# Optimization experiments

Measured on AMD Instinct MI355X. Metric: run time of the kernel, lower is better.

## Reference

```python
import jax, jax.numpy as jnp
import numpy as np

EPS = 1e-5
NEG_SLOPE = 0.01  # torch LeakyReLU default


def setup_inputs() -> dict:
    key = jax.random.key(0)
    k1, k2 = jax.random.split(key)
    B, C, N, OUT = 4, 256, 4096, 256
    stdv = 1.0 / np.sqrt(OUT)
    x = jax.random.normal(k1, (B, C, N), dtype=jnp.float32)
    W = jax.random.uniform(k2, (C, OUT), dtype=jnp.float32, minval=-stdv, maxval=stdv)
    gamma = jnp.ones((OUT,), dtype=jnp.float32)
    beta = jnp.zeros((OUT,), dtype=jnp.float32)
    return {"x": x, "W": W, "gamma": gamma, "beta": beta}


def reference(x, W, gamma, beta):
    # x: [B, C, N] -> xt: [B, N, C]
    xt = jnp.transpose(x, (0, 2, 1))
    # adjacency: softmax over last dim of [B, N, N] self-similarity (L2=False path)
    scores = jnp.einsum('bnc,bmc->bnm', xt, xt)
    adj = jax.nn.softmax(scores, axis=-1)
    # support: [B, N, OUT]
    support = jnp.einsum('bnc,co->bno', xt, W)
    # output: [B, OUT, N]
    out = jnp.transpose(jnp.einsum('bnm,bmo->bno', adj, support), (0, 2, 1))
    y = jnp.where(out >= 0, out, NEG_SLOPE * out)  # LeakyReLU
    # BatchNorm1d (training mode): per-channel stats over batch and spatial dims
    mean = jnp.mean(y, axis=(0, 2), keepdims=True)
    var = jnp.mean(jnp.square(y - mean), axis=(0, 2), keepdims=True)
    y_hat = (y - mean) * jax.lax.rsqrt(var + EPS)
    return gamma[None, :, None] * y_hat + beta[None, :, None]
```

## Files before the change

### kernel.cpp

```cpp
#include <hip/hip_runtime.h>

typedef _Float16 f16;
typedef _Float16 f16x2 __attribute__((ext_vector_type(2)));
typedef _Float16 f16x4 __attribute__((ext_vector_type(4)));
typedef _Float16 f16x8 __attribute__((ext_vector_type(8)));
typedef float f32x4 __attribute__((ext_vector_type(4)));
typedef float f32x16 __attribute__((ext_vector_type(16)));
typedef int i32x2 __attribute__((ext_vector_type(2)));

#define B_   4
#define C_   256
#define N_   4096
#define OUT_ 256

__device__ __forceinline__ void gld_lds16(const f16* g, f16* l) {
    __builtin_amdgcn_global_load_lds(
        (const __attribute__((address_space(1))) void*)g,
        (__attribute__((address_space(3))) void*)l, 16, 0, 0);
}

__device__ __forceinline__ i32x2 perm32(float x) {
    return __builtin_amdgcn_permlane32_swap(__float_as_int(x), __float_as_int(x), false, false);
}

__global__ __launch_bounds__(256) void k_prep(const float* __restrict__ x,
                                              const float* __restrict__ W,
                                              f16* __restrict__ xt,
                                              f16* __restrict__ Wt,
                                              float* __restrict__ stats) {
    int bid = blockIdx.x;
    int t = threadIdx.x;
    if (bid < 1024) {
        int b  = bid >> 8;
        int ct = (bid >> 6) & 3;
        int nt = bid & 63;
        int c0 = ct * 64, n0 = nt * 64;
        __shared__ float tile[64][65];
        int nl = t & 63;
        int r0 = t >> 6;
        #pragma unroll
        for (int i = 0; i < 16; ++i) {
            int cl = i * 4 + r0;
            tile[cl][nl] = x[((b * C_ + c0 + cl) * N_) + n0 + nl];
        }
        __syncthreads();
        #pragma unroll
        for (int i = 0; i < 4; ++i) {
            int n  = i * 16 + (t >> 4);
            int c4 = (t & 15) * 4;
            f16x4 o = { (f16)tile[c4][n], (f16)tile[c4 + 1][n],
                        (f16)tile[c4 + 2][n], (f16)tile[c4 + 3][n] };
            *(f16x4*)&xt[((b * N_ + n0 + n) * C_) + c0 + c4] = o;
        }
    } else {
        int wb = bid - 1024;
        #pragma unroll
        for (int i = 0; i < 4; ++i) {
            int idx = wb * 1024 + i * 256 + t;
            int c = idx >> 8, o = idx & 255;
            Wt[o * C_ + c] = (f16)W[idx];
        }
        if (wb < 2) stats[wb * 256 + t] = 0.f;
    }
}

__global__ __launch_bounds__(256) void k_support(const f16* __restrict__ xt,
                                                 const f16* __restrict__ Wt,
                                                 f16* __restrict__ supT) {
    int bid0 = blockIdx.x;
    int bid = (bid0 & 7) * 128 + (bid0 >> 3);
    int b  = bid >> 8;
    int ot = (bid >> 6) & 3;
    int mt = bid & 63;
    int o0 = ot * 64, m0 = mt * 64;
    __shared__ __align__(16) f16 Ws[64][264];
    __shared__ __align__(16) f16 Xs[64][264];
    int t = threadIdx.x;
    int wave = t >> 6, lane = t & 63, q = lane >> 4, l15 = lane & 15;
    #pragma unroll
    for (int p = 0; p < 8; ++p) {
        int idx = p * 256 + t;
        int row = idx >> 5, ch = (idx & 31) * 8;
        *(uint4*)&Ws[row][ch] = *(const uint4*)&Wt[(o0 + row) * C_ + ch];
        *(uint4*)&Xs[row][ch] = *(const uint4*)&xt[((b * N_) + m0 + row) * C_ + ch];
    }
    __syncthreads();
    f32x4 acc[4] = {};
    #pragma unroll
    for (int kk = 0; kk < 8; ++kk) {
        f16x8 a = *(f16x8*)&Ws[16 * wave + l15][kk * 32 + q * 8];
        #pragma unroll
        for (int ct = 0; ct < 4; ++ct) {
            f16x8 bb = *(f16x8*)&Xs[16 * ct + l15][kk * 32 + q * 8];
            acc[ct] = __builtin_amdgcn_mfma_f32_16x16x32_f16(a, bb, acc[ct], 0, 0, 0);
        }
    }
    #pragma unroll
    for (int ct = 0; ct < 4; ++ct)
        #pragma unroll
        for (int r = 0; r < 4; ++r) {
            int og = o0 + 16 * wave + q * 4 + r;
            int mg = m0 + 16 * ct + l15;
            supT[((b * OUT_ + og) * N_) + mg] = (f16)acc[ct][r];
        }
}

__global__ __launch_bounds__(256) __attribute__((amdgpu_waves_per_eu(2, 2)))
void k_flash(const f16* __restrict__ xt,
             const f16* __restrict__ supT,
             f16* __restrict__ Op,
             float* __restrict__ Ml) {
    int bid0 = blockIdx.x;
    int wg = (bid0 & 7) * 64 + (bid0 >> 3);
    int h  = wg >> 8;
    int b  = (wg >> 6) & 3;
    int n0 = (wg & 63) * 64;

    __shared__ __align__(16) f16 KsL[64 * 256];
    __shared__ __align__(16) f16 Ps[64][72];
    __shared__ float Lh[2][64];
    __shared__ float Lt[64];

    int t = threadIdx.x;
    int wave = t >> 6, lane = t & 63;
    int q = lane >> 4, l15 = lane & 15;
    int l31 = lane & 31, hi = lane >> 5;
    int nh = wave & 1, mh = wave >> 1;

    const f16* qbase = xt + ((size_t)(b * N_) + n0 + 32 * nh + l31) * C_ + 8 * hi;
    f16x8 qf[16];
    #pragma unroll
    for (int kc = 0; kc < 16; ++kc)
        qf[kc] = *(const f16x8*)&qbase[16 * kc];

    float m_fix;
    {
        float s = 0.f;
        #pragma unroll
        for (int kc = 0; kc < 16; ++kc)
            #pragma unroll
            for (int j = 0; j < 8; ++j) {
                float v = (float)qf[kc][j];
                s += v * v;
            }
        i32x2 rr = perm32(s);
        m_fix = __int_as_float(rr[0]) + __int_as_float(rr[1]);
    }

    f32x4 oacc[4][4] = {};
    float l_run = 0.f;

    const f16* kbase = xt + (size_t)b * N_ * C_;
    int c16 = (lane & 31) * 8;
    int rhalf = lane >> 5;
    int soff[8];
    #pragma unroll
    for (int j = 0; j < 8; ++j) {
        int row = wave * 16 + j * 2 + rhalf;
        soff[j] = row * 256 + (c16 ^ ((row & 7) << 3));
    }
    int swr = (l31 & 7) << 3;

    const f16* vbbase = supT + ((size_t)(b * OUT_) + 64 * wave + l15) * N_ + q * 8;

    {
        const f16* kt = kbase + (size_t)(h * 2048) * C_;
        #pragma unroll
        for (int j = 0; j < 8; ++j)
            gld_lds16(kt + soff[j], &KsL[wave * 4096 + j * 512]);
    }

    for (int it = 0; it < 32; ++it) {
        int m0 = h * 2048 + it * 64;

        asm volatile("s_waitcnt vmcnt(0) lgkmcnt(0)" ::: "memory");
        __builtin_amdgcn_s_barrier();
        __builtin_amdgcn_sched_barrier(0);

        f16x8 vf[2][4];
        const f16* vb = vbbase + m0;
        #pragma unroll
        for (int ks = 0; ks < 2; ++ks)
            #pragma unroll
            for (int ot = 0; ot < 4; ++ot)
                vf[ks][ot] = *(const f16x8*)&vb[(size_t)(16 * ot) * N_ + ks * 32];

        f32x16 sacc = {};
        const f16* krow = &KsL[(32 * mh + l31) * 256];
        __builtin_amdgcn_s_setprio(1);
        #pragma unroll
        for (int kc = 0; kc < 16; ++kc) {
            int col = (16 * kc + 8 * hi) ^ swr;
            f16x8 kf = *(const f16x8*)&krow[col];
            sacc = __builtin_amdgcn_mfma_f32_32x32x16_f16(kf, qf[kc], sacc, 0, 0, 0);
        }
        __builtin_amdgcn_s_setprio(0);

        float p[16];
        #pragma unroll
        for (int r = 0; r < 16; ++r)
            p[r] = __expf(sacc[r] - m_fix);
        float s0 = (p[0] + p[1]) + (p[2] + p[3]);
        float s1 = (p[4] + p[5]) + (p[6] + p[7]);
        float s2 = (p[8] + p[9]) + (p[10] + p[11]);
        float s3 = (p[12] + p[13]) + (p[14] + p[15]);
        l_run += (s0 + s1) + (s2 + s3);

        #pragma unroll
        for (int g = 0; g < 4; ++g) {
            f16x4 pk = { (f16)p[4 * g], (f16)p[4 * g + 1],
                         (f16)p[4 * g + 2], (f16)p[4 * g + 3] };
            *(f16x4*)&Ps[32 * nh + l31][32 * mh + 8 * g + 4 * hi] = pk;
        }

        asm volatile("s_waitcnt lgkmcnt(0)" ::: "memory");
        __builtin_amdgcn_s_barrier();
        __builtin_amdgcn_sched_barrier(0);

        if (it < 31) {
            const f16* kt = kbase + (size_t)(m0 + 64) * C_;
            #pragma unroll
            for (int j = 0; j < 8; ++j)
                gld_lds16(kt + soff[j], &KsL[wave * 4096 + j * 512]);
        }

        __builtin_amdgcn_s_setprio(1);
        #pragma unroll
        for (int ks = 0; ks < 2; ++ks) {
            f16x8 af[4];
            #pragma unroll
            for (int nt = 0; nt < 4; ++nt)
                af[nt] = *(f16x8*)&Ps[16 * nt + l15][ks * 32 + q * 8];
            #pragma unroll
            for (int nt = 0; nt < 4; ++nt)
                #pragma unroll
                for (int ot = 0; ot < 4; ++ot)
                    oacc[nt][ot] = __builtin_amdgcn_mfma_f32_16x16x32_f16(af[nt], vf[ks][ot], oacc[nt][ot], 0, 0, 0);
        }
        __builtin_amdgcn_s_setprio(0);
    }

    {
        i32x2 rr = perm32(l_run);
        l_run = __int_as_float(rr[0]) + __int_as_float(rr[1]);
    }
    __syncthreads();
    if (lane < 32) Lh[mh][32 * nh + l31] = l_run;
    __syncthreads();
    if (t < 64) {
        float lt = Lh[0][t] + Lh[1][t];
        Lt[t] = 1.0f / fmaxf(lt, 1e-37f);
        Ml[(size_t)wg * 64 + t] = lt;
    }
    __syncthreads();

    float4 lv[4];
    #pragma unroll
    for (int nt = 0; nt < 4; ++nt)
        lv[nt] = *(const float4*)&Lt[16 * nt + 4 * q];

    f16* Obase = Op + (size_t)wg * (64 * 256);
    #pragma unroll
    for (int nt = 0; nt < 4; ++nt)
        #pragma unroll
        for (int ot = 0; ot < 4; ++ot)
            #pragma unroll
            for (int r = 0; r < 4; ++r) {
                int n = 16 * nt + q * 4 + r;
                int o = 64 * wave + 16 * ot + l15;
                Obase[n * 256 + o] = (f16)(oacc[nt][ot][r] * ((const float*)&lv[nt])[r]);
            }
}

__global__ __launch_bounds__(256) void k_merge(const f16* __restrict__ Op,
                                               const float* __restrict__ Ml,
                                               float* __restrict__ out,
                                               float* __restrict__ stats) {
    int bid0 = blockIdx.x;
    int bid = (bid0 & 7) * 128 + (bid0 >> 3);
    int b  = bid >> 8;
    int nb = (bid >> 2) & 63;
    int oq = bid & 3;
    int n0 = nb * 64, o0 = oq * 64;
    int t = threadIdx.x;
    const f16* O1 = Op + (size_t)(b * 64 + nb) * (64 * 256);
    const f16* O2 = Op + (size_t)(b * 64 + nb + 256) * (64 * 256);
    const float* Ml1 = Ml + (size_t)(b * 64 + nb) * 64;
    const float* Ml2 = Ml + (size_t)(b * 64 + nb + 256) * 64;
    __shared__ float c1s[64], c2s[64];
    __shared__ float tile[64][65];
    __shared__ float rs[8][64], rss[8][64];
    if (t < 64) {
        float l1 = Ml1[t], l2 = Ml2[t];
        float inv = 1.0f / (l1 + l2);
        c1s[t] = l1 * inv;
        c2s[t] = l2 * inv;
    }
    __syncthreads();
    int ow = (t & 31) * 2;
    int ng = t >> 5;
    float s0 = 0.f, s1 = 0.f, ss0 = 0.f, ss1 = 0.f;
    #pragma unroll
    for (int j = 0; j < 8; ++j) {
        int n = ng * 8 + j;
        f16x2 u1 = *(const f16x2*)&O1[n * 256 + o0 + ow];
        f16x2 u2 = *(const f16x2*)&O2[n * 256 + o0 + ow];
        float c1 = c1s[n], c2 = c2s[n];
        float v0 = c1 * (float)u1[0] + c2 * (float)u2[0];
        float v1 = c1 * (float)u1[1] + c2 * (float)u2[1];
        v0 = v0 >= 0.f ? v0 : 0.01f * v0;
        v1 = v1 >= 0.f ? v1 : 0.01f * v1;
        s0 += v0; ss0 += v0 * v0;
        s1 += v1; ss1 += v1 * v1;
        tile[ow][n] = v0;
        tile[ow + 1][n] = v1;
    }
    rs[ng][ow] = s0;  rs[ng][ow + 1] = s1;
    rss[ng][ow] = ss0; rss[ng][ow + 1] = ss1;
    __syncthreads();
    if (t < 64) {
        float S = 0.f, SS = 0.f;
        #pragma unroll
        for (int g = 0; g < 8; ++g) { S += rs[g][t]; SS += rss[g][t]; }
        atomicAdd(&stats[o0 + t], S);
        atomicAdd(&stats[256 + o0 + t], SS);
    }
    int w = t >> 6, lane = t & 63;
    float* dst = out + ((size_t)(b * OUT_ + o0)) * N_ + n0;
    #pragma unroll
    for (int k = 0; k < 16; ++k) {
        int o = 16 * w + k;
        dst[(size_t)o * N_ + lane] = tile[o][lane];
    }
}

__global__ __launch_bounds__(256) void k_bnapply(float* __restrict__ y,
                                                 const float* __restrict__ stats,
                                                 const float* __restrict__ gamma,
                                                 const float* __restrict__ beta) {
    int idx = blockIdx.x * 256 + threadIdx.x;
    int o = (idx >> 10) & 255;
    float mean = stats[o] * (1.0f / 16384.0f);
    float var = stats[256 + o] * (1.0f / 16384.0f) - mean * mean;
    float rstd = rsqrtf(var + 1e-5f);
    float g = gamma[o] * rstd;
    float bta = beta[o] - mean * g;
    float4 v = ((const float4*)y)[idx];
    v.x = v.x * g + bta;
    v.y = v.y * g + bta;
    v.z = v.z * g + bta;
    v.w = v.w * g + bta;
    ((float4*)y)[idx] = v;
}

extern "C" void kernel_launch(void* const* d_in, const int* in_sizes, int n_in,
                              void* d_out, int out_size, void* d_ws, size_t ws_size,
                              hipStream_t stream) {
    const float* x     = (const float*)d_in[0];
    const float* W     = (const float*)d_in[1];
    const float* gamma = (const float*)d_in[2];
    const float* beta  = (const float*)d_in[3];
    float* out = (float*)d_out;

    f16* xt    = (f16*)d_ws;
    f16* supT  = xt + (size_t)B_ * N_ * C_;
    f16* Wt    = supT + (size_t)B_ * N_ * OUT_;
    f16* Op    = Wt + C_ * OUT_;
    float* Ml  = (float*)(Op + (size_t)2 * 256 * 64 * 256);
    float* stats = Ml + 512 * 128;

    k_prep<<<1088, 256, 0, stream>>>(x, W, xt, Wt, stats);
    k_support<<<1024, 256, 0, stream>>>(xt, Wt, supT);
    k_flash<<<512, 256, 0, stream>>>(xt, supT, Op, Ml);
    k_merge<<<1024, 256, 0, stream>>>(Op, Ml, out, stats);
    k_bnapply<<<4096, 256, 0, stream>>>(out, stats, gamma, beta);
}
```

Before: 191.6 us.

## Split flash attention keys four ways with workspace-gated fallback double-buffered path

Adds a four-way split-K variant of the flash kernel (1024 blocks over 1024-key halves, waves_per_eu relaxed to 2-4) with a four-way merge kernel, selected when the workspace is large enough. The split aims to improve CU occupancy and load balance on the attention stage. It costs twice the partial-output traffic and a heavier merge. The fallback path keeps the two-way split but double-buffers the K tile in LDS, so the next tile's load overlaps compute.

```diff
diff --git a/kernel.cpp b/kernel.cpp
--- a/kernel.cpp
+++ b/kernel.cpp
@@ -105,13 +105,13 @@
         }
 }
 
-__global__ __launch_bounds__(256) __attribute__((amdgpu_waves_per_eu(2, 2)))
-void k_flash(const f16* __restrict__ xt,
-             const f16* __restrict__ supT,
-             f16* __restrict__ Op,
-             float* __restrict__ Ml) {
+__global__ __launch_bounds__(256) __attribute__((amdgpu_waves_per_eu(2, 4)))
+void k_flash4(const f16* __restrict__ xt,
+              const f16* __restrict__ supT,
+              f16* __restrict__ Op,
+              float* __restrict__ Ml) {
     int bid0 = blockIdx.x;
-    int wg = (bid0 & 7) * 64 + (bid0 >> 3);
+    int wg = (bid0 & 7) * 128 + (bid0 >> 3);
     int h  = wg >> 8;
     int b  = (wg >> 6) & 3;
     int n0 = (wg & 63) * 64;
@@ -164,14 +164,14 @@
     const f16* vbbase = supT + ((size_t)(b * OUT_) + 64 * wave + l15) * N_ + q * 8;
 
     {
-        const f16* kt = kbase + (size_t)(h * 2048) * C_;
+        const f16* kt = kbase + (size_t)(h * 1024) * C_;
         #pragma unroll
         for (int j = 0; j < 8; ++j)
             gld_lds16(kt + soff[j], &KsL[wave * 4096 + j * 512]);
     }
 
-    for (int it = 0; it < 32; ++it) {
-        int m0 = h * 2048 + it * 64;
+    for (int it = 0; it < 16; ++it) {
+        int m0 = h * 1024 + it * 64;
 
         asm volatile("s_waitcnt vmcnt(0) lgkmcnt(0)" ::: "memory");
         __builtin_amdgcn_s_barrier();
@@ -217,7 +217,7 @@
         __builtin_amdgcn_s_barrier();
         __builtin_amdgcn_sched_barrier(0);
 
-        if (it < 31) {
+        if (it < 15) {
             const f16* kt = kbase + (size_t)(m0 + 64) * C_;
             #pragma unroll
             for (int j = 0; j < 8; ++j)
@@ -272,10 +272,246 @@
             }
 }
 
-__global__ __launch_bounds__(256) void k_merge(const f16* __restrict__ Op,
-                                               const float* __restrict__ Ml,
-                                               float* __restrict__ out,
-                                               float* __restrict__ stats) {
+__global__ __launch_bounds__(256) __attribute__((amdgpu_waves_per_eu(2, 2)))
+void k_flash2(const f16* __restrict__ xt,
+              const f16* __restrict__ supT,
+              f16* __restrict__ Op,
+              float* __restrict__ Ml) {
+    int bid0 = blockIdx.x;
+    int wg = (bid0 & 7) * 64 + (bid0 >> 3);
+    int h  = wg >> 8;
+    int b  = (wg >> 6) & 3;
+    int n0 = (wg & 63) * 64;
+
+    __shared__ __align__(16) f16 KsL[2][64 * 256];
+    __shared__ __align__(16) f16 Ps[64][72];
+    __shared__ float Lh[2][64];
+    __shared__ float Lt[64];
+
+    int t = threadIdx.x;
+    int wave = t >> 6, lane = t & 63;
+    int q = lane >> 4, l15 = lane & 15;
+    int l31 = lane & 31, hi = lane >> 5;
+    int nh = wave & 1, mh = wave >> 1;
+
+    const f16* qbase = xt + ((size_t)(b * N_) + n0 + 32 * nh + l31) * C_ + 8 * hi;
+    f16x8 qf[16];
+    #pragma unroll
+    for (int kc = 0; kc < 16; ++kc)
+        qf[kc] = *(const f16x8*)&qbase[16 * kc];
+
+    float m_fix;
+    {
+        float s = 0.f;
+        #pragma unroll
+        for (int kc = 0; kc < 16; ++kc)
+            #pragma unroll
+            for (int j = 0; j < 8; ++j) {
+                float v = (float)qf[kc][j];
+                s += v * v;
+            }
+        i32x2 rr = perm32(s);
+        m_fix = __int_as_float(rr[0]) + __int_as_float(rr[1]);
+    }
+
+    f32x4 oacc[4][4] = {};
+    float l_run = 0.f;
+
+    const f16* kbase = xt + (size_t)b * N_ * C_;
+    int c16 = (lane & 31) * 8;
+    int rhalf = lane >> 5;
+    int soff[8];
+    #pragma unroll
+    for (int j = 0; j < 8; ++j) {
+        int row = wave * 16 + j * 2 + rhalf;
+        soff[j] = row * 256 + (c16 ^ ((row & 7) << 3));
+    }
+    int swr = (l31 & 7) << 3;
+
+    const f16* vbbase = supT + ((size_t)(b * OUT_) + 64 * wave + l15) * N_ + q * 8;
+
+    {
+        const f16* kt = kbase + (size_t)(h * 2048) * C_;
+        #pragma unroll
+        for (int j = 0; j < 8; ++j)
+            gld_lds16(kt + soff[j], &KsL[0][wave * 4096 + j * 512]);
+    }
+
+    int cur = 0;
+    for (int it = 0; it < 32; ++it) {
+        int m0 = h * 2048 + it * 64;
+        __syncthreads();
+
+        f16x8 vf[2][4];
+        const f16* vb = vbbase + m0;
+        #pragma unroll
+        for (int ks = 0; ks < 2; ++ks)
+            #pragma unroll
+            for (int ot = 0; ot < 4; ++ot)
+                vf[ks][ot] = *(const f16x8*)&vb[(size_t)(16 * ot) * N_ + ks * 32];
+
+        if (it < 31) {
+            const f16* kt = kbase + (size_t)(m0 + 64) * C_;
+            #pragma unroll
+            for (int j = 0; j < 8; ++j)
+                gld_lds16(kt + soff[j], &KsL[cur ^ 1][wave * 4096 + j * 512]);
+        }
+
+        f32x16 sacc = {};
+        const f16* krow = &KsL[cur][(32 * mh + l31) * 256];
+        __builtin_amdgcn_s_setprio(1);
+        #pragma unroll
+        for (int kc = 0; kc < 16; ++kc) {
+            int col = (16 * kc + 8 * hi) ^ swr;
+            f16x8 kf = *(const f16x8*)&krow[col];
+            sacc = __builtin_amdgcn_mfma_f32_32x32x16_f16(kf, qf[kc], sacc, 0, 0, 0);
+        }
+        __builtin_amdgcn_s_setprio(0);
+
+        float p[16];
+        #pragma unroll
+        for (int r = 0; r < 16; ++r)
+            p[r] = __expf(sacc[r] - m_fix);
+        float s0 = (p[0] + p[1]) + (p[2] + p[3]);
+        float s1 = (p[4] + p[5]) + (p[6] + p[7]);
+        float s2 = (p[8] + p[9]) + (p[10] + p[11]);
+        float s3 = (p[12] + p[13]) + (p[14] + p[15]);
+        l_run += (s0 + s1) + (s2 + s3);
+
+        #pragma unroll
+        for (int g = 0; g < 4; ++g) {
+            f16x4 pk = { (f16)p[4 * g], (f16)p[4 * g + 1],
+                         (f16)p[4 * g + 2], (f16)p[4 * g + 3] };
+            *(f16x4*)&Ps[32 * nh + l31][32 * mh + 8 * g + 4 * hi] = pk;
+        }
+
+        asm volatile("s_waitcnt lgkmcnt(0)" ::: "memory");
+        __builtin_amdgcn_s_barrier();
+        __builtin_amdgcn_sched_barrier(0);
+
+        __builtin_amdgcn_s_setprio(1);
+        #pragma unroll
+        for (int ks = 0; ks < 2; ++ks) {
+            f16x8 af[4];
+            #pragma unroll
+            for (int nt = 0; nt < 4; ++nt)
+                af[nt] = *(f16x8*)&Ps[16 * nt + l15][ks * 32 + q * 8];
+            #pragma unroll
+            for (int nt = 0; nt < 4; ++nt)
+                #pragma unroll
+                for (int ot = 0; ot < 4; ++ot)
+                    oacc[nt][ot] = __builtin_amdgcn_mfma_f32_16x16x32_f16(af[nt], vf[ks][ot], oacc[nt][ot], 0, 0, 0);
+        }
+        __builtin_amdgcn_s_setprio(0);
+        cur ^= 1;
+    }
+
+    {
+        i32x2 rr = perm32(l_run);
+        l_run = __int_as_float(rr[0]) + __int_as_float(rr[1]);
+    }
+    __syncthreads();
+    if (lane < 32) Lh[mh][32 * nh + l31] = l_run;
+    __syncthreads();
+    if (t < 64) {
+        float lt = Lh[0][t] + Lh[1][t];
+        Lt[t] = 1.0f / fmaxf(lt, 1e-37f);
+        Ml[(size_t)wg * 64 + t] = lt;
+    }
+    __syncthreads();
+
+    float4 lv[4];
+    #pragma unroll
+    for (int nt = 0; nt < 4; ++nt)
+        lv[nt] = *(const float4*)&Lt[16 * nt + 4 * q];
+
+    f16* Obase = Op + (size_t)wg * (64 * 256);
+    #pragma unroll
+    for (int nt = 0; nt < 4; ++nt)
+        #pragma unroll
+        for (int ot = 0; ot < 4; ++ot)
+            #pragma unroll
+            for (int r = 0; r < 4; ++r) {
+                int n = 16 * nt + q * 4 + r;
+                int o = 64 * wave + 16 * ot + l15;
+                Obase[n * 256 + o] = (f16)(oacc[nt][ot][r] * ((const float*)&lv[nt])[r]);
+            }
+}
+
+__global__ __launch_bounds__(256) void k_merge4(const f16* __restrict__ Op,
+                                                const float* __restrict__ Ml,
+                                                float* __restrict__ out,
+                                                float* __restrict__ stats) {
+    int bid0 = blockIdx.x;
+    int bid = (bid0 & 7) * 128 + (bid0 >> 3);
+    int b  = bid >> 8;
+    int nb = (bid >> 2) & 63;
+    int oq = bid & 3;
+    int n0 = nb * 64, o0 = oq * 64;
+    int t = threadIdx.x;
+    const f16* Oh[4];
+    #pragma unroll
+    for (int hh = 0; hh < 4; ++hh)
+        Oh[hh] = Op + (size_t)(hh * 256 + b * 64 + nb) * (64 * 256);
+    __shared__ float cs[4][64];
+    __shared__ float tile[64][65];
+    __shared__ float rs[8][64], rss[8][64];
+    if (t < 64) {
+        float l0 = Ml[(size_t)(0 * 256 + b * 64 + nb) * 64 + t];
+        float l1 = Ml[(size_t)(1 * 256 + b * 64 + nb) * 64 + t];
+        float l2 = Ml[(size_t)(2 * 256 + b * 64 + nb) * 64 + t];
+        float l3 = Ml[(size_t)(3 * 256 + b * 64 + nb) * 64 + t];
+        float inv = 1.0f / (l0 + l1 + l2 + l3);
+        cs[0][t] = l0 * inv;
+        cs[1][t] = l1 * inv;
+        cs[2][t] = l2 * inv;
+        cs[3][t] = l3 * inv;
+    }
+    __syncthreads();
+    int ow = (t & 31) * 2;
+    int ng = t >> 5;
+    float s0 = 0.f, s1 = 0.f, ss0 = 0.f, ss1 = 0.f;
+    #pragma unroll
+    for (int j = 0; j < 8; ++j) {
+        int n = ng * 8 + j;
+        float v0 = 0.f, v1 = 0.f;
+        #pragma unroll
+        for (int hh = 0; hh < 4; ++hh) {
+            f16x2 u = *(const f16x2*)&Oh[hh][n * 256 + o0 + ow];
+            float c = cs[hh][n];
+            v0 += c * (float)u[0];
+            v1 += c * (float)u[1];
+        }
+        v0 = v0 >= 0.f ? v0 : 0.01f * v0;
+        v1 = v1 >= 0.f ? v1 : 0.01f * v1;
+        s0 += v0; ss0 += v0 * v0;
+        s1 += v1; ss1 += v1 * v1;
+        tile[ow][n] = v0;
+        tile[ow + 1][n] = v1;
+    }
+    rs[ng][ow] = s0;  rs[ng][ow + 1] = s1;
+    rss[ng][ow] = ss0; rss[ng][ow + 1] = ss1;
+    __syncthreads();
+    if (t < 64) {
+        float S = 0.f, SS = 0.f;
+        #pragma unroll
+        for (int g = 0; g < 8; ++g) { S += rs[g][t]; SS += rss[g][t]; }
+        atomicAdd(&stats[o0 + t], S);
+        atomicAdd(&stats[256 + o0 + t], SS);
+    }
+    int w = t >> 6, lane = t & 63;
+    float* dst = out + ((size_t)(b * OUT_ + o0)) * N_ + n0;
+    #pragma unroll
+    for (int k = 0; k < 16; ++k) {
+        int o = 16 * w + k;
+        dst[(size_t)o * N_ + lane] = tile[o][lane];
+    }
+}
+
+__global__ __launch_bounds__(256) void k_merge2(const f16* __restrict__ Op,
+                                                const float* __restrict__ Ml,
+                                                float* __restrict__ out,
+                                                float* __restrict__ stats) {
     int bid0 = blockIdx.x;
     int bid = (bid0 & 7) * 128 + (bid0 >> 3);
     int b  = bid >> 8;
@@ -362,16 +598,29 @@
     const float* beta  = (const float*)d_in[3];
     float* out = (float*)d_out;
 
-    f16* xt    = (f16*)d_ws;
-    f16* supT  = xt + (size_t)B_ * N_ * C_;
-    f16* Wt    = supT + (size_t)B_ * N_ * OUT_;
-    f16* Op    = Wt + C_ * OUT_;
-    float* Ml  = (float*)(Op + (size_t)2 * 256 * 64 * 256);
-    float* stats = Ml + 512 * 128;
-
-    k_prep<<<1088, 256, 0, stream>>>(x, W, xt, Wt, stats);
-    k_support<<<1024, 256, 0, stream>>>(xt, Wt, supT);
-    k_flash<<<512, 256, 0, stream>>>(xt, supT, Op, Ml);
-    k_merge<<<1024, 256, 0, stream>>>(Op, Ml, out, stats);
-    k_bnapply<<<4096, 256, 0, stream>>>(out, stats, gamma, beta);
-}
+    f16* xt   = (f16*)d_ws;
+    f16* supT = xt + (size_t)B_ * N_ * C_;
+    f16* Wt   = supT + (size_t)B_ * N_ * OUT_;
+    f16* Op   = Wt + C_ * OUT_;
+
+    size_t need4 = (size_t)(8 + 8 + 32) * 1024 * 1024 + 131072 * 2 + 262144 + 2048;
+    bool four = ws_size >= need4;
+
+    if (four) {
+        float* Ml    = (float*)(Op + (size_t)4 * 256 * 64 * 256);
+        float* stats = Ml + (size_t)1024 * 64;
+        k_prep<<<1088, 256, 0, stream>>>(x, W, xt, Wt, stats);
+        k_support<<<1024, 256, 0, stream>>>(xt, Wt, supT);
+        k_flash4<<<1024, 256, 0, stream>>>(xt, supT, Op, Ml);
+        k_merge4<<<1024, 256, 0, stream>>>(Op, Ml, out, stats);
+        k_bnapply<<<4096, 256, 0, stream>>>(out, stats, gamma, beta);
+    } else {
+        float* Ml    = (float*)(Op + (size_t)2 * 256 * 64 * 256);
+        float* stats = Ml + (size_t)512 * 128;
+        k_prep<<<1088, 256, 0, stream>>>(x, W, xt, Wt, stats);
+        k_support<<<1024, 256, 0, stream>>>(xt, Wt, supT);
+        k_flash2<<<512, 256, 0, stream>>>(xt, supT, Op, Ml);
+        k_merge2<<<1024, 256, 0, stream>>>(Op, Ml, out, stats);
+        k_bnapply<<<4096, 256, 0, stream>>>(out, stats, gamma, beta);
+    }
+}
```

After: 200.0 us. +4.4%, slower.
